# Performance work log

Measured on AMD Instinct MI355X. Metric: run time of the kernel, lower is better.

The kernel has to match this reference:

```python
import jax, jax.numpy as jnp
import numpy as np

D_MODEL, H, D_K = 768, 12, 64
B, S = 2, 2048
NEG = -1.0e9


def setup_inputs() -> dict:
    key = jax.random.key(0)
    ks = jax.random.split(key, 7)
    q = jax.random.normal(ks[0], (B, S, D_MODEL), dtype=jnp.float32)
    k = jax.random.normal(ks[1], (B, S, D_MODEL), dtype=jnp.float32)
    v = jax.random.normal(ks[2], (B, S, D_MODEL), dtype=jnp.float32)
    mask = jnp.tril(jnp.ones((S, S), dtype=jnp.int32))[None, None]  # [1,1,S,S] causal
    sc = 1.0 / np.sqrt(D_MODEL)
    w_q = jax.random.normal(ks[3], (D_MODEL, D_MODEL), dtype=jnp.float32) * sc
    w_k = jax.random.normal(ks[4], (D_MODEL, D_MODEL), dtype=jnp.float32) * sc
    w_v = jax.random.normal(ks[5], (D_MODEL, D_MODEL), dtype=jnp.float32) * sc
    w_o = jax.random.normal(ks[6], (D_MODEL, D_MODEL), dtype=jnp.float32) * sc
    return {"q": q, "k": k, "v": v, "mask": mask,
            "w_q": w_q, "w_k": w_k, "w_v": w_v, "w_o": w_o}


def reference(q, k, v, mask, w_q, w_k, w_v, w_o):
    # nn.Linear(x) = x @ W.T ; split heads: [B,S,D] -> [B,H,S,Dk]
    def split_heads(x, w):
        y = jnp.einsum('bsd,ed->bse', x, w)
        return y.reshape(x.shape[0], x.shape[1], H, D_K).transpose(0, 2, 1, 3)

    qh = split_heads(q, w_q)
    kh = split_heads(k, w_k)
    vh = split_heads(v, w_v)
    scores = jnp.einsum('bhqd,bhkd->bhqk', qh, kh) / jnp.sqrt(jnp.float32(D_K))
    scores = jnp.where(mask == 0, jnp.float32(NEG), scores)
    attn = jax.nn.softmax(scores, axis=-1)  # dropout p=0 -> identity
    ctx = jnp.einsum('bhqk,bhkd->bhqd', attn, vh)
    ctx = ctx.transpose(0, 2, 1, 3).reshape(q.shape[0], q.shape[1], D_MODEL)
    return jnp.einsum('bsd,ed->bse', ctx, w_o)
```

## Files before the change

kernel.cpp:

```cpp
#include <hip/hip_runtime.h>

#define DM   768
#define HN   12
#define DKH  64
#define BSZ  2
#define SEQ  2048
#define MROWS (BSZ*SEQ)
#define NEGBIG -1.0e9f
#define NSLOT 40
#define QSCALE 0.18033688011112042f

typedef __bf16 bf16;
typedef __bf16 bf16x8 __attribute__((ext_vector_type(8)));
typedef __bf16 bf16x4 __attribute__((ext_vector_type(4)));
typedef float  f32x4  __attribute__((ext_vector_type(4)));
typedef unsigned int uint32;

__device__ __forceinline__ void gload_lds16(const void* g, void* l) {
    __builtin_amdgcn_global_load_lds(
        (const __attribute__((address_space(1))) char*)g,
        (__attribute__((address_space(3))) char*)l, 16, 0, 0);
}

__global__ __launch_bounds__(256) void cvt4(const float* __restrict__ a, const float* __restrict__ b,
                                            const float* __restrict__ c, const float* __restrict__ e,
                                            bf16* __restrict__ x, bf16* __restrict__ y,
                                            bf16* __restrict__ z, bf16* __restrict__ u, int n) {
    const float* s; bf16* d;
    if      (blockIdx.y == 0) { s = a; d = x; }
    else if (blockIdx.y == 1) { s = b; d = y; }
    else if (blockIdx.y == 2) { s = c; d = z; }
    else                      { s = e; d = u; }
    int i = (blockIdx.x * 256 + threadIdx.x) * 4;
    if (i + 3 < n) {
        float4 v = *(const float4*)(s + i);
        bf16x4 o; o[0] = (bf16)v.x; o[1] = (bf16)v.y; o[2] = (bf16)v.z; o[3] = (bf16)v.w;
        *(bf16x4*)(d + i) = o;
    }
}

__global__ __launch_bounds__(256) void gemm_qkv(
    const float* __restrict__ xq, const float* __restrict__ xk, const float* __restrict__ xv,
    const bf16* __restrict__ wq, const bf16* __restrict__ wk, const bf16* __restrict__ wv,
    bf16* __restrict__ qh, bf16* __restrict__ kh, bf16* __restrict__ vt)
{
    __shared__ float Asf[128 * 32];
    __shared__ bf16  Bs[128 * 32];

    const float* A; const bf16* Bw; bf16* Out; float qs;
    if      (blockIdx.z == 0) { A = xq; Bw = wq; Out = qh; qs = QSCALE; }
    else if (blockIdx.z == 1) { A = xk; Bw = wk; Out = kh; qs = 1.0f; }
    else                      { A = xv; Bw = wv; Out = vt; qs = 1.0f; }
    const bool vout = (blockIdx.z == 2);

    const int t = threadIdx.x, w = t >> 6, lane = t & 63;
    const int g = lane >> 4, lo = lane & 15;
    const int mt = blockIdx.x * 128, nt = blockIdx.y * 128;
    const int wr = (w >> 1) * 64, wc = (w & 1) * 64;

    f32x4 acc[4][4] = {};

    for (int k0 = 0; k0 < DM; k0 += 32) {
        #pragma unroll
        for (int i = 0; i < 4; i++) {
            int c = i * 256 + t;
            int row = c >> 3, cc = (c & 7) ^ (row & 7);
            gload_lds16(A + (size_t)(mt + row) * DM + k0 + cc * 4, (char*)Asf + c * 16);
        }
        #pragma unroll
        for (int i = 0; i < 2; i++) {
            int c = i * 256 + t;
            int row = c >> 2, col = (c & 3) * 8;
            gload_lds16(Bw + (size_t)(nt + row) * DM + k0 + col, (char*)Bs + c * 16);
        }
        asm volatile("s_waitcnt vmcnt(0)" ::: "memory");
        __syncthreads();

        bf16x8 af[4], bfr[4];
        #pragma unroll
        for (int m = 0; m < 4; m++) {
            int row = wr + m * 16 + lo;
            const char* rp = (const char*)Asf + row * 128;
            float4 f0 = *(const float4*)(rp + (((2 * g)     ^ (lo & 7)) << 4));
            float4 f1 = *(const float4*)(rp + (((2 * g + 1) ^ (lo & 7)) << 4));
            bf16x8 a;
            a[0] = (bf16)f0.x; a[1] = (bf16)f0.y; a[2] = (bf16)f0.z; a[3] = (bf16)f0.w;
            a[4] = (bf16)f1.x; a[5] = (bf16)f1.y; a[6] = (bf16)f1.z; a[7] = (bf16)f1.w;
            af[m] = a;
        }
        #pragma unroll
        for (int n = 0; n < 4; n++)
            bfr[n] = *(const bf16x8*)&Bs[(wc + n * 16 + lo) * 32 + g * 8];
        #pragma unroll
        for (int m = 0; m < 4; m++)
            #pragma unroll
            for (int n = 0; n < 4; n++)
                acc[m][n] = __builtin_amdgcn_mfma_f32_16x16x32_bf16(af[m], bfr[n], acc[m][n], 0, 0, 0);
        __syncthreads();
    }

    if (!vout) {
        #pragma unroll
        for (int m = 0; m < 4; m++) {
            #pragma unroll
            for (int n = 0; n < 4; n++) {
                #pragma unroll
                for (int r = 0; r < 4; r++) {
                    int gm = mt + wr + m * 16 + g * 4 + r;
                    int gn = nt + wc + n * 16 + lo;
                    int b = gm >> 11, s = gm & 2047, h = gn >> 6, d = gn & 63;
                    Out[(((size_t)b * HN + h) * SEQ + s) * DKH + d] = (bf16)(acc[m][n][r] * qs);
                }
            }
        }
    } else {
        #pragma unroll
        for (int m = 0; m < 4; m++) {
            #pragma unroll
            for (int n = 0; n < 4; n++) {
                int gm = mt + wr + m * 16 + g * 4;
                int gn = nt + wc + n * 16 + lo;
                int b = gm >> 11, s0 = gm & 2047, h = gn >> 6, d = gn & 63;
                bf16x4 pk;
                #pragma unroll
                for (int r = 0; r < 4; r++) pk[r] = (bf16)acc[m][n][r];
                *(bf16x4*)&Out[(((size_t)b * HN + h) * DKH + d) * SEQ + s0] = pk;
            }
        }
    }
}

__global__ __launch_bounds__(256) void gemm_out(
    const bf16* __restrict__ Actx, const bf16* __restrict__ Bw, float* __restrict__ Out)
{
    __shared__ bf16 As[128 * 32];
    __shared__ bf16 Bs[128 * 32];

    const int t = threadIdx.x, w = t >> 6, lane = t & 63;
    const int mt = blockIdx.x * 128, nt = blockIdx.y * 128;
    const int wr = (w >> 1) * 64, wc = (w & 1) * 64;

    f32x4 acc[4][4] = {};

    for (int k0 = 0; k0 < DM; k0 += 32) {
        #pragma unroll
        for (int i = 0; i < 2; i++) {
            int c = i * 256 + t;
            int row = c >> 2, col = (c & 3) * 8;
            gload_lds16(Actx + (size_t)(mt + row) * DM + k0 + col, (char*)As + c * 16);
            gload_lds16(Bw   + (size_t)(nt + row) * DM + k0 + col, (char*)Bs + c * 16);
        }
        asm volatile("s_waitcnt vmcnt(0)" ::: "memory");
        __syncthreads();

        bf16x8 af[4], bfr[4];
        #pragma unroll
        for (int m = 0; m < 4; m++)
            af[m] = *(const bf16x8*)&As[(wr + m * 16 + (lane & 15)) * 32 + (lane >> 4) * 8];
        #pragma unroll
        for (int n = 0; n < 4; n++)
            bfr[n] = *(const bf16x8*)&Bs[(wc + n * 16 + (lane & 15)) * 32 + (lane >> 4) * 8];
        #pragma unroll
        for (int m = 0; m < 4; m++)
            #pragma unroll
            for (int n = 0; n < 4; n++)
                acc[m][n] = __builtin_amdgcn_mfma_f32_16x16x32_bf16(af[m], bfr[n], acc[m][n], 0, 0, 0);
        __syncthreads();
    }

    #pragma unroll
    for (int m = 0; m < 4; m++) {
        #pragma unroll
        for (int n = 0; n < 4; n++) {
            #pragma unroll
            for (int r = 0; r < 4; r++) {
                int gm = mt + wr + m * 16 + (lane >> 4) * 4 + r;
                int gn = nt + wc + n * 16 + (lane & 15);
                Out[(size_t)gm * DM + gn] = acc[m][n][r];
            }
        }
    }
}

__global__ __launch_bounds__(256, 4) void flash_split(
    const bf16* __restrict__ qh, const bf16* __restrict__ kh,
    const bf16* __restrict__ vt, bf16* __restrict__ ctx,
    bf16* __restrict__ pO, float* __restrict__ pM, float* __restrict__ pL)
{
    __shared__ bf16 Ks[2][4096];
    __shared__ bf16 Vs[2][4096];
    __shared__ bf16 pl[4][1024];

    const int bid = blockIdx.x;
    const int slot = bid / 24;
    const int bh = bid % 24;

    int qt, p, np;
    if (slot < 16)      { qt = 15 - (slot >> 2); p = slot & 3;  np = 4; }
    else if (slot < 28) { int s = slot - 16; qt = 11 - s / 3; p = s % 3; np = 3; }
    else if (slot < 36) { int s = slot - 28; qt = 7 - (s >> 1); p = s & 1; np = 2; }
    else                { qt = 39 - slot; p = 0; np = 1; }

    const int T = 2 * qt + 2;
    const int bse = T / np, rem = T - bse * np;
    const int cnt   = bse + (p < rem ? 1 : 0);
    const int start = p * bse + (p < rem ? p : rem);

    const int qb = qt * 128;
    const int t = threadIdx.x, w = t >> 6, lane = t & 63;
    const int g = lane >> 4, lo = lane & 15;
    const size_t base = (size_t)bh * SEQ * DKH;
    const char* khead = (const char*)(kh + base);
    const char* vhead = (const char*)(vt + base);

    uint32 koff[2], voff[2];
    #pragma unroll
    for (int i = 0; i < 2; i++) {
        int c = w * 128 + i * 64 + lane;
        int r = c >> 3, s = c & 7;
        int sw = s ^ (r & 7);
        koff[i] = (uint32)(r * 128  + 16 * sw);
        voff[i] = (uint32)(r * 4096 + 16 * sw);
    }
    const uint32 kr0 = (uint32)(128 * lo + 16 * (g ^ (lo & 7)));
    const uint32 kr1 = kr0 ^ 64;

    uint32 pw[4], pr[2];
    #pragma unroll
    for (int cg = 0; cg < 4; cg++)
        pw[cg] = (uint32)(lo * 128 + (((2 * cg + (g >> 1)) ^ (lo & 7)) << 4) + (g & 1) * 8);
    #pragma unroll
    for (int kq = 0; kq < 2; kq++)
        pr[kq] = (uint32)(lo * 128 + (((4 * kq + g) ^ (lo & 7)) << 4));
    char* plb = (char*)&pl[w][0];

    const int qrow0 = qb + 16 * w + lo;
    const int qrow1 = qb + 64 + 16 * w + lo;
    const bf16* qp0 = qh + base + (size_t)qrow0 * DKH + g * 8;
    const bf16* qp1 = qh + base + (size_t)qrow1 * DKH + g * 8;
    bf16x8 qa0 = *(const bf16x8*)qp0;
    bf16x8 qa1 = *(const bf16x8*)(qp0 + 32);
    bf16x8 qb0 = *(const bf16x8*)qp1;
    bf16x8 qb1 = *(const bf16x8*)(qp1 + 32);

    f32x4 O0[4] = {}, O1[4] = {};
    float m0 = -1e30f, l0 = 0.0f, m1 = -1e30f, l1 = 0.0f;

    #pragma unroll
    for (int i = 0; i < 2; i++) {
        int c16 = (w * 128 + i * 64 + lane) * 16;
        gload_lds16(khead + (size_t)start * 8192 + koff[i], (char*)&Ks[0][0] + c16);
        gload_lds16(vhead + (size_t)start * 128  + voff[i], (char*)&Vs[0][0] + c16);
    }
    asm volatile("s_waitcnt vmcnt(0)" ::: "memory");
    __syncthreads();

    for (int it = 0; it < cnt; ++it) {
        const int kt = start + it;
        const int par = it & 1, nxt = par ^ 1;
        if (it + 1 < cnt) {
            const char* ks = khead + (size_t)(kt + 1) * 8192;
            const char* vs = vhead + (size_t)(kt + 1) * 128;
            #pragma unroll
            for (int i = 0; i < 2; i++) {
                int c16 = (w * 128 + i * 64 + lane) * 16;
                gload_lds16(ks + koff[i], (char*)&Ks[nxt][0] + c16);
                gload_lds16(vs + voff[i], (char*)&Vs[nxt][0] + c16);
            }
        }

        const bool act0  = (kt != T - 1);
        const bool diag0 = (kt == T - 2);
        const bool diag1 = (kt == T - 1);

        const char* Kp = (const char*)&Ks[par][0];
        f32x4 s0[4], s1[4];
        {
            bf16x8 kf0[4], kf1[4];
            #pragma unroll
            for (int cg = 0; cg < 4; cg++) {
                kf0[cg] = *(const bf16x8*)(Kp + cg * 2048 + kr0);
                kf1[cg] = *(const bf16x8*)(Kp + cg * 2048 + kr1);
            }
            __builtin_amdgcn_s_setprio(1);
            if (act0) {
                #pragma unroll
                for (int cg = 0; cg < 4; cg++) {
                    f32x4 z = {0.0f, 0.0f, 0.0f, 0.0f};
                    z = __builtin_amdgcn_mfma_f32_16x16x32_bf16(kf0[cg], qa0, z, 0, 0, 0);
                    z = __builtin_amdgcn_mfma_f32_16x16x32_bf16(kf1[cg], qa1, z, 0, 0, 0);
                    s0[cg] = z;
                }
            }
            #pragma unroll
            for (int cg = 0; cg < 4; cg++) {
                f32x4 z = {0.0f, 0.0f, 0.0f, 0.0f};
                z = __builtin_amdgcn_mfma_f32_16x16x32_bf16(kf0[cg], qb0, z, 0, 0, 0);
                z = __builtin_amdgcn_mfma_f32_16x16x32_bf16(kf1[cg], qb1, z, 0, 0, 0);
                s1[cg] = z;
            }
            __builtin_amdgcn_s_setprio(0);
        }

        if (act0 && diag0) {
            #pragma unroll
            for (int cg = 0; cg < 4; cg++)
                #pragma unroll
                for (int r = 0; r < 4; r++) {
                    int ki = kt * 64 + cg * 16 + 4 * g + r;
                    s0[cg][r] = (ki > qrow0) ? NEGBIG : s0[cg][r];
                }
        }
        if (diag1) {
            #pragma unroll
            for (int cg = 0; cg < 4; cg++)
                #pragma unroll
                for (int r = 0; r < 4; r++) {
                    int ki = kt * 64 + cg * 16 + 4 * g + r;
                    s1[cg][r] = (ki > qrow1) ? NEGBIG : s1[cg][r];
                }
        }

        if (act0) {
            float mx = fmaxf(fmaxf(fmaxf(s0[0][0], s0[0][1]), fmaxf(s0[0][2], s0[0][3])),
                             fmaxf(fmaxf(s0[1][0], s0[1][1]), fmaxf(s0[1][2], s0[1][3])));
            mx = fmaxf(mx, fmaxf(fmaxf(fmaxf(s0[2][0], s0[2][1]), fmaxf(s0[2][2], s0[2][3])),
                                 fmaxf(fmaxf(s0[3][0], s0[3][1]), fmaxf(s0[3][2], s0[3][3]))));
            mx = fmaxf(mx, __shfl_xor(mx, 16, 64));
            mx = fmaxf(mx, __shfl_xor(mx, 32, 64));
            if (!__all(mx - m0 <= 8.0f)) {
                float mnew = fmaxf(m0, mx);
                float scl = __builtin_exp2f(m0 - mnew);
                m0 = mnew; l0 *= scl;
                float s4[4];
                #pragma unroll
                for (int r = 0; r < 4; r++) s4[r] = __shfl(scl, 4 * g + r, 64);
                #pragma unroll
                for (int dg = 0; dg < 4; dg++)
                    #pragma unroll
                    for (int r = 0; r < 4; r++) O0[dg][r] *= s4[r];
            }
            float rs = 0.0f;
            #pragma unroll
            for (int cg = 0; cg < 4; cg++)
                #pragma unroll
                for (int r = 0; r < 4; r++) {
                    s0[cg][r] = __builtin_exp2f(s0[cg][r] - m0);
                    rs += s0[cg][r];
                }
            rs += __shfl_xor(rs, 16, 64);
            rs += __shfl_xor(rs, 32, 64);
            l0 += rs;
        }
        {
            float mx = fmaxf(fmaxf(fmaxf(s1[0][0], s1[0][1]), fmaxf(s1[0][2], s1[0][3])),
                             fmaxf(fmaxf(s1[1][0], s1[1][1]), fmaxf(s1[1][2], s1[1][3])));
            mx = fmaxf(mx, fmaxf(fmaxf(fmaxf(s1[2][0], s1[2][1]), fmaxf(s1[2][2], s1[2][3])),
                                 fmaxf(fmaxf(s1[3][0], s1[3][1]), fmaxf(s1[3][2], s1[3][3]))));
            mx = fmaxf(mx, __shfl_xor(mx, 16, 64));
            mx = fmaxf(mx, __shfl_xor(mx, 32, 64));
            if (!__all(mx - m1 <= 8.0f)) {
                float mnew = fmaxf(m1, mx);
                float scl = __builtin_exp2f(m1 - mnew);
                m1 = mnew; l1 *= scl;
                float s4[4];
                #pragma unroll
                for (int r = 0; r < 4; r++) s4[r] = __shfl(scl, 4 * g + r, 64);
                #pragma unroll
                for (int dg = 0; dg < 4; dg++)
                    #pragma unroll
                    for (int r = 0; r < 4; r++) O1[dg][r] *= s4[r];
            }
            float rs = 0.0f;
            #pragma unroll
            for (int cg = 0; cg < 4; cg++)
                #pragma unroll
                for (int r = 0; r < 4; r++) {
                    s1[cg][r] = __builtin_exp2f(s1[cg][r] - m1);
                    rs += s1[cg][r];
                }
            rs += __shfl_xor(rs, 16, 64);
            rs += __shfl_xor(rs, 32, 64);
            l1 += rs;
        }

        const char* Vp = (const char*)&Vs[par][0];
        bf16x8 vv[8];
        #pragma unroll
        for (int kq = 0; kq < 2; kq++)
            #pragma unroll
            for (int dblk = 0; dblk < 4; dblk++)
                vv[kq * 4 + dblk] = *(const bf16x8*)
                    (Vp + (dblk * 16 + lo) * 128 + 16 * ((4 * kq + g) ^ (lo & 7)));

        if (act0) {
            #pragma unroll
            for (int cg = 0; cg < 4; cg++) {
                bf16x4 pk;
                #pragma unroll
                for (int r = 0; r < 4; r++) pk[r] = (bf16)s0[cg][r];
                *(bf16x4*)(plb + pw[cg]) = pk;
            }
        }
        asm volatile("s_waitcnt lgkmcnt(0)" ::: "memory");
        __builtin_amdgcn_sched_barrier(0);
        if (act0) {
            __builtin_amdgcn_s_setprio(1);
            #pragma unroll
            for (int kq = 0; kq < 2; kq++) {
                bf16x8 pa = *(const bf16x8*)(plb + pr[kq]);
                #pragma unroll
                for (int dblk = 0; dblk < 4; dblk++)
                    O0[dblk] = __builtin_amdgcn_mfma_f32_16x16x32_bf16(pa, vv[kq * 4 + dblk], O0[dblk], 0, 0, 0);
            }
            __builtin_amdgcn_s_setprio(0);
        }
        __builtin_amdgcn_sched_barrier(0);
        {
            #pragma unroll
            for (int cg = 0; cg < 4; cg++) {
                bf16x4 pk;
                #pragma unroll
                for (int r = 0; r < 4; r++) pk[r] = (bf16)s1[cg][r];
                *(bf16x4*)(plb + pw[cg]) = pk;
            }
            asm volatile("s_waitcnt lgkmcnt(0)" ::: "memory");
            __builtin_amdgcn_sched_barrier(0);
            __builtin_amdgcn_s_setprio(1);
            #pragma unroll
            for (int kq = 0; kq < 2; kq++) {
                bf16x8 pa = *(const bf16x8*)(plb + pr[kq]);
                #pragma unroll
                for (int dblk = 0; dblk < 4; dblk++)
                    O1[dblk] = __builtin_amdgcn_mfma_f32_16x16x32_bf16(pa, vv[kq * 4 + dblk], O1[dblk], 0, 0, 0);
            }
            __builtin_amdgcn_s_setprio(0);
        }

        asm volatile("s_waitcnt vmcnt(0)" ::: "memory");
        __syncthreads();
    }

    if (np == 1) {
        const int b = bh / HN, h = bh % HN;
        float inv0[4], inv1[4];
        #pragma unroll
        for (int r = 0; r < 4; r++) {
            inv0[r] = 1.0f / __shfl(l0, 4 * g + r, 64);
            inv1[r] = 1.0f / __shfl(l1, 4 * g + r, 64);
        }
        #pragma unroll
        for (int dg = 0; dg < 4; dg++) {
            #pragma unroll
            for (int r = 0; r < 4; r++) {
                int row0 = qb + 16 * w + g * 4 + r;
                int row1 = qb + 64 + 16 * w + g * 4 + r;
                ctx[((size_t)(b * SEQ + row0)) * DM + h * DKH + dg * 16 + lo] =
                    (bf16)(O0[dg][r] * inv0[r]);
                ctx[((size_t)(b * SEQ + row1)) * DM + h * DKH + dg * 16 + lo] =
                    (bf16)(O1[dg][r] * inv1[r]);
            }
        }
    } else {
        const int pslot = bh * NSLOT + slot;
        bf16* po = pO + (size_t)pslot * 128 * 64;
        #pragma unroll
        for (int dg = 0; dg < 4; dg++) {
            #pragma unroll
            for (int r = 0; r < 4; r++) {
                int r0 = 16 * w + 4 * g + r;
                po[r0 * 64 + dg * 16 + lo]        = (bf16)O0[dg][r];
                po[(64 + r0) * 64 + dg * 16 + lo] = (bf16)O1[dg][r];
            }
        }
        if (g == 0) {
            pM[pslot * 128 + 16 * w + lo]      = m0;
            pL[pslot * 128 + 16 * w + lo]      = l0;
            pM[pslot * 128 + 64 + 16 * w + lo] = m1;
            pL[pslot * 128 + 64 + 16 * w + lo] = l1;
        }
    }
}

__global__ __launch_bounds__(256) void flash_combine(
    const bf16* __restrict__ pO, const float* __restrict__ pM,
    const float* __restrict__ pL, bf16* __restrict__ ctx)
{
    const int bh = blockIdx.x;
    const int qt = 4 + blockIdx.y;
    int np, s0;
    if (qt >= 12)     { np = 4; s0 = (15 - qt) * 4; }
    else if (qt >= 8) { np = 3; s0 = 16 + (11 - qt) * 3; }
    else              { np = 2; s0 = 28 + (7 - qt) * 2; }

    const int t = threadIdx.x;
    const int row = t >> 1, dh = (t & 1) * 32;
    const int pbase = bh * NSLOT + s0;

    float mi[4], wi[4];
    float mstar = -1e30f;
    #pragma unroll
    for (int i = 0; i < 4; i++)
        if (i < np) { mi[i] = pM[(pbase + i) * 128 + row]; mstar = fmaxf(mstar, mi[i]); }
    float lsum = 0.0f;
    #pragma unroll
    for (int i = 0; i < 4; i++)
        if (i < np) { wi[i] = __builtin_exp2f(mi[i] - mstar); lsum += wi[i] * pL[(pbase + i) * 128 + row]; }
    const float linv = 1.0f / lsum;

    const int b = bh / HN, h = bh % HN;
    bf16* crow = ctx + ((size_t)(b * SEQ + qt * 128 + row)) * DM + h * DKH + dh;

    #pragma unroll
    for (int d0 = 0; d0 < 32; d0 += 8) {
        float acc[8] = {};
        #pragma unroll
        for (int i = 0; i < 4; i++) {
            if (i < np) {
                bf16x8 o = *(const bf16x8*)&pO[((size_t)(pbase + i) * 128 + row) * 64 + dh + d0];
                #pragma unroll
                for (int j = 0; j < 8; j++) acc[j] += wi[i] * (float)o[j];
            }
        }
        bf16x8 ov;
        #pragma unroll
        for (int j = 0; j < 8; j++) ov[j] = (bf16)(acc[j] * linv);
        *(bf16x8*)(crow + d0) = ov;
    }
}

extern "C" void kernel_launch(void* const* d_in, const int* in_sizes, int n_in,
                              void* d_out, int out_size, void* d_ws, size_t ws_size,
                              hipStream_t stream) {
    const float* q  = (const float*)d_in[0];
    const float* k  = (const float*)d_in[1];
    const float* v  = (const float*)d_in[2];
    const float* wq = (const float*)d_in[4];
    const float* wk = (const float*)d_in[5];
    const float* wv = (const float*)d_in[6];
    const float* wo = (const float*)d_in[7];
    float* out = (float*)d_out;

    const size_t NX = (size_t)MROWS * DM;
    const size_t NW = (size_t)DM * DM;

    bf16* p = (bf16*)d_ws;
    bf16* wqb = p; p += NW;
    bf16* wkb = p; p += NW;
    bf16* wvb = p; p += NW;
    bf16* wob = p; p += NW;
    bf16* qhp = p; p += NX;
    bf16* khp = p; p += NX;
    bf16* vtp = p; p += NX;
    bf16* ctxp = p; p += NX;
    bf16* pO = p; p += (size_t)24 * NSLOT * 128 * 64;
    float* pM = (float*)p;
    float* pL = pM + 24 * NSLOT * 128;

    cvt4<<<dim3(NW / 1024, 4), 256, 0, stream>>>(wq, wk, wv, wo, wqb, wkb, wvb, wob, (int)NW);

    gemm_qkv<<<dim3(MROWS / 128, DM / 128, 3), 256, 0, stream>>>(
        q, k, v, wqb, wkb, wvb, qhp, khp, vtp);

    flash_split<<<24 * NSLOT, 256, 0, stream>>>(qhp, khp, vtp, ctxp, pO, pM, pL);
    flash_combine<<<dim3(24, 12), 256, 0, stream>>>(pO, pM, pL, ctxp);

    gemm_out<<<dim3(MROWS / 128, DM / 128), 256, 0, stream>>>(ctxp, wob, out);
}
```

Before: 118.5 us.

## Fuse weight fp32-to-bf16 conversion into GEMM tile loads, drop cvt4 kernel

Removes the separate weight conversion kernel and has the QKV and output GEMMs load fp32 weight tiles into LDS (swizzled like the activation tiles) and convert to bf16 in registers. This saves one kernel launch and the round trip of the converted weights through memory. In exchange it doubles LDS traffic and footprint for the B tiles and adds conversion work inside every k-step. It also lowers the flash_split occupancy hint from 4 to 3 blocks per CU.

```diff
diff --git a/kernel.cpp b/kernel.cpp
--- a/kernel.cpp
+++ b/kernel.cpp
@@ -22,32 +22,15 @@
         (__attribute__((address_space(3))) char*)l, 16, 0, 0);
 }
 
-__global__ __launch_bounds__(256) void cvt4(const float* __restrict__ a, const float* __restrict__ b,
-                                            const float* __restrict__ c, const float* __restrict__ e,
-                                            bf16* __restrict__ x, bf16* __restrict__ y,
-                                            bf16* __restrict__ z, bf16* __restrict__ u, int n) {
-    const float* s; bf16* d;
-    if      (blockIdx.y == 0) { s = a; d = x; }
-    else if (blockIdx.y == 1) { s = b; d = y; }
-    else if (blockIdx.y == 2) { s = c; d = z; }
-    else                      { s = e; d = u; }
-    int i = (blockIdx.x * 256 + threadIdx.x) * 4;
-    if (i + 3 < n) {
-        float4 v = *(const float4*)(s + i);
-        bf16x4 o; o[0] = (bf16)v.x; o[1] = (bf16)v.y; o[2] = (bf16)v.z; o[3] = (bf16)v.w;
-        *(bf16x4*)(d + i) = o;
-    }
-}
-
 __global__ __launch_bounds__(256) void gemm_qkv(
     const float* __restrict__ xq, const float* __restrict__ xk, const float* __restrict__ xv,
-    const bf16* __restrict__ wq, const bf16* __restrict__ wk, const bf16* __restrict__ wv,
+    const float* __restrict__ wq, const float* __restrict__ wk, const float* __restrict__ wv,
     bf16* __restrict__ qh, bf16* __restrict__ kh, bf16* __restrict__ vt)
 {
     __shared__ float Asf[128 * 32];
-    __shared__ bf16  Bs[128 * 32];
-
-    const float* A; const bf16* Bw; bf16* Out; float qs;
+    __shared__ float Bsf[128 * 32];
+
+    const float* A; const float* Bw; bf16* Out; float qs;
     if      (blockIdx.z == 0) { A = xq; Bw = wq; Out = qh; qs = QSCALE; }
     else if (blockIdx.z == 1) { A = xk; Bw = wk; Out = kh; qs = 1.0f; }
     else                      { A = xv; Bw = wv; Out = vt; qs = 1.0f; }
@@ -65,13 +48,8 @@
         for (int i = 0; i < 4; i++) {
             int c = i * 256 + t;
             int row = c >> 3, cc = (c & 7) ^ (row & 7);
-            gload_lds16(A + (size_t)(mt + row) * DM + k0 + cc * 4, (char*)Asf + c * 16);
-        }
-        #pragma unroll
-        for (int i = 0; i < 2; i++) {
-            int c = i * 256 + t;
-            int row = c >> 2, col = (c & 3) * 8;
-            gload_lds16(Bw + (size_t)(nt + row) * DM + k0 + col, (char*)Bs + c * 16);
+            gload_lds16(A  + (size_t)(mt + row) * DM + k0 + cc * 4, (char*)Asf + c * 16);
+            gload_lds16(Bw + (size_t)(nt + row) * DM + k0 + cc * 4, (char*)Bsf + c * 16);
         }
         asm volatile("s_waitcnt vmcnt(0)" ::: "memory");
         __syncthreads();
@@ -79,8 +57,7 @@
         bf16x8 af[4], bfr[4];
         #pragma unroll
         for (int m = 0; m < 4; m++) {
-            int row = wr + m * 16 + lo;
-            const char* rp = (const char*)Asf + row * 128;
+            const char* rp = (const char*)Asf + (wr + m * 16 + lo) * 128;
             float4 f0 = *(const float4*)(rp + (((2 * g)     ^ (lo & 7)) << 4));
             float4 f1 = *(const float4*)(rp + (((2 * g + 1) ^ (lo & 7)) << 4));
             bf16x8 a;
@@ -89,8 +66,15 @@
             af[m] = a;
         }
         #pragma unroll
-        for (int n = 0; n < 4; n++)
-            bfr[n] = *(const bf16x8*)&Bs[(wc + n * 16 + lo) * 32 + g * 8];
+        for (int n = 0; n < 4; n++) {
+            const char* rp = (const char*)Bsf + (wc + n * 16 + lo) * 128;
+            float4 f0 = *(const float4*)(rp + (((2 * g)     ^ (lo & 7)) << 4));
+            float4 f1 = *(const float4*)(rp + (((2 * g + 1) ^ (lo & 7)) << 4));
+            bf16x8 b;
+            b[0] = (bf16)f0.x; b[1] = (bf16)f0.y; b[2] = (bf16)f0.z; b[3] = (bf16)f0.w;
+            b[4] = (bf16)f1.x; b[5] = (bf16)f1.y; b[6] = (bf16)f1.z; b[7] = (bf16)f1.w;
+            bfr[n] = b;
+        }
         #pragma unroll
         for (int m = 0; m < 4; m++)
             #pragma unroll
@@ -131,12 +115,13 @@
 }
 
 __global__ __launch_bounds__(256) void gemm_out(
-    const bf16* __restrict__ Actx, const bf16* __restrict__ Bw, float* __restrict__ Out)
+    const bf16* __restrict__ Actx, const float* __restrict__ Bw, float* __restrict__ Out)
 {
-    __shared__ bf16 As[128 * 32];
-    __shared__ bf16 Bs[128 * 32];
+    __shared__ bf16  As[128 * 32];
+    __shared__ float Bsf[128 * 32];
 
     const int t = threadIdx.x, w = t >> 6, lane = t & 63;
+    const int g = lane >> 4, lo = lane & 15;
     const int mt = blockIdx.x * 128, nt = blockIdx.y * 128;
     const int wr = (w >> 1) * 64, wc = (w & 1) * 64;
 
@@ -148,7 +133,12 @@
             int c = i * 256 + t;
             int row = c >> 2, col = (c & 3) * 8;
             gload_lds16(Actx + (size_t)(mt + row) * DM + k0 + col, (char*)As + c * 16);
-            gload_lds16(Bw   + (size_t)(nt + row) * DM + k0 + col, (char*)Bs + c * 16);
+        }
+        #pragma unroll
+        for (int i = 0; i < 4; i++) {
+            int c = i * 256 + t;
+            int row = c >> 3, cc = (c & 7) ^ (row & 7);
+            gload_lds16(Bw + (size_t)(nt + row) * DM + k0 + cc * 4, (char*)Bsf + c * 16);
         }
         asm volatile("s_waitcnt vmcnt(0)" ::: "memory");
         __syncthreads();
@@ -156,10 +146,17 @@
         bf16x8 af[4], bfr[4];
         #pragma unroll
         for (int m = 0; m < 4; m++)
-            af[m] = *(const bf16x8*)&As[(wr + m * 16 + (lane & 15)) * 32 + (lane >> 4) * 8];
-        #pragma unroll
-        for (int n = 0; n < 4; n++)
-            bfr[n] = *(const bf16x8*)&Bs[(wc + n * 16 + (lane & 15)) * 32 + (lane >> 4) * 8];
+            af[m] = *(const bf16x8*)&As[(wr + m * 16 + lo) * 32 + g * 8];
+        #pragma unroll
+        for (int n = 0; n < 4; n++) {
+            const char* rp = (const char*)Bsf + (wc + n * 16 + lo) * 128;
+            float4 f0 = *(const float4*)(rp + (((2 * g)     ^ (lo & 7)) << 4));
+            float4 f1 = *(const float4*)(rp + (((2 * g + 1) ^ (lo & 7)) << 4));
+            bf16x8 b;
+            b[0] = (bf16)f0.x; b[1] = (bf16)f0.y; b[2] = (bf16)f0.z; b[3] = (bf16)f0.w;
+            b[4] = (bf16)f1.x; b[5] = (bf16)f1.y; b[6] = (bf16)f1.z; b[7] = (bf16)f1.w;
+            bfr[n] = b;
+        }
         #pragma unroll
         for (int m = 0; m < 4; m++)
             #pragma unroll
@@ -174,15 +171,15 @@
         for (int n = 0; n < 4; n++) {
             #pragma unroll
             for (int r = 0; r < 4; r++) {
-                int gm = mt + wr + m * 16 + (lane >> 4) * 4 + r;
-                int gn = nt + wc + n * 16 + (lane & 15);
+                int gm = mt + wr + m * 16 + g * 4 + r;
+                int gn = nt + wc + n * 16 + lo;
                 Out[(size_t)gm * DM + gn] = acc[m][n][r];
             }
         }
     }
 }
 
-__global__ __launch_bounds__(256, 4) void flash_split(
+__global__ __launch_bounds__(256, 3) void flash_split(
     const bf16* __restrict__ qh, const bf16* __restrict__ kh,
     const bf16* __restrict__ vt, bf16* __restrict__ ctx,
     bf16* __restrict__ pO, float* __restrict__ pM, float* __restrict__ pL)
@@ -542,13 +539,8 @@
     float* out = (float*)d_out;
 
     const size_t NX = (size_t)MROWS * DM;
-    const size_t NW = (size_t)DM * DM;
 
     bf16* p = (bf16*)d_ws;
-    bf16* wqb = p; p += NW;
-    bf16* wkb = p; p += NW;
-    bf16* wvb = p; p += NW;
-    bf16* wob = p; p += NW;
     bf16* qhp = p; p += NX;
     bf16* khp = p; p += NX;
     bf16* vtp = p; p += NX;
@@ -557,13 +549,11 @@
     float* pM = (float*)p;
     float* pL = pM + 24 * NSLOT * 128;
 
-    cvt4<<<dim3(NW / 1024, 4), 256, 0, stream>>>(wq, wk, wv, wo, wqb, wkb, wvb, wob, (int)NW);
-
     gemm_qkv<<<dim3(MROWS / 128, DM / 128, 3), 256, 0, stream>>>(
-        q, k, v, wqb, wkb, wvb, qhp, khp, vtp);
+        q, k, v, wq, wk, wv, qhp, khp, vtp);
 
     flash_split<<<24 * NSLOT, 256, 0, stream>>>(qhp, khp, vtp, ctxp, pO, pM, pL);
     flash_combine<<<dim3(24, 12), 256, 0, stream>>>(pO, pM, pL, ctxp);
 
-    gemm_out<<<dim3(MROWS / 128, DM / 128), 256, 0, stream>>>(ctxp, wob, out);
+    gemm_out<<<dim3(MROWS / 128, DM / 128), 256, 0, stream>>>(ctxp, wo, out);
 }
```

After: 116.3 us. No clear change (-1.8%).

## Double-buffer GEMM tiles and convert output weights to bf16 on the fly in LDS

Applied to the files above, without the earlier changes.

Both projection GEMMs now keep two LDS buffers and issue the next k-tile's global-to-LDS loads before computing the current one, so load latency overlaps with MFMA work. The output projection reads fp32 w_o directly through a swizzled LDS layout and converts it to bf16 during fragment loads, which drops the fourth conversion pass and its workspace. The flash kernel's launch-bounds occupancy hint is lowered from 4 to 3 blocks. The extra buffers double LDS use per GEMM block, which may reduce how many blocks fit on each CU.

```diff
diff --git a/kernel.cpp b/kernel.cpp
--- a/kernel.cpp
+++ b/kernel.cpp
@@ -44,8 +44,8 @@
     const bf16* __restrict__ wq, const bf16* __restrict__ wk, const bf16* __restrict__ wv,
     bf16* __restrict__ qh, bf16* __restrict__ kh, bf16* __restrict__ vt)
 {
-    __shared__ float Asf[128 * 32];
-    __shared__ bf16  Bs[128 * 32];
+    __shared__ float Asf[2][128 * 32];
+    __shared__ bf16  Bs[2][128 * 32];
 
     const float* A; const bf16* Bw; bf16* Out; float qs;
     if      (blockIdx.z == 0) { A = xq; Bw = wq; Out = qh; qs = QSCALE; }
@@ -60,27 +60,45 @@
 
     f32x4 acc[4][4] = {};
 
-    for (int k0 = 0; k0 < DM; k0 += 32) {
-        #pragma unroll
-        for (int i = 0; i < 4; i++) {
-            int c = i * 256 + t;
-            int row = c >> 3, cc = (c & 7) ^ (row & 7);
-            gload_lds16(A + (size_t)(mt + row) * DM + k0 + cc * 4, (char*)Asf + c * 16);
-        }
-        #pragma unroll
-        for (int i = 0; i < 2; i++) {
-            int c = i * 256 + t;
-            int row = c >> 2, col = (c & 3) * 8;
-            gload_lds16(Bw + (size_t)(nt + row) * DM + k0 + col, (char*)Bs + c * 16);
-        }
-        asm volatile("s_waitcnt vmcnt(0)" ::: "memory");
-        __syncthreads();
+    const int NT = DM / 32;
+
+    #pragma unroll
+    for (int i = 0; i < 4; i++) {
+        int c = i * 256 + t;
+        int row = c >> 3, cc = (c & 7) ^ (row & 7);
+        gload_lds16(A + (size_t)(mt + row) * DM + cc * 4, (char*)&Asf[0][0] + c * 16);
+    }
+    #pragma unroll
+    for (int i = 0; i < 2; i++) {
+        int c = i * 256 + t;
+        int row = c >> 2, col = (c & 3) * 8;
+        gload_lds16(Bw + (size_t)(nt + row) * DM + col, (char*)&Bs[0][0] + c * 16);
+    }
+    asm volatile("s_waitcnt vmcnt(0)" ::: "memory");
+    __syncthreads();
+
+    for (int it = 0; it < NT; ++it) {
+        const int par = it & 1, nxt = par ^ 1;
+        if (it + 1 < NT) {
+            int k0 = (it + 1) * 32;
+            #pragma unroll
+            for (int i = 0; i < 4; i++) {
+                int c = i * 256 + t;
+                int row = c >> 3, cc = (c & 7) ^ (row & 7);
+                gload_lds16(A + (size_t)(mt + row) * DM + k0 + cc * 4, (char*)&Asf[nxt][0] + c * 16);
+            }
+            #pragma unroll
+            for (int i = 0; i < 2; i++) {
+                int c = i * 256 + t;
+                int row = c >> 2, col = (c & 3) * 8;
+                gload_lds16(Bw + (size_t)(nt + row) * DM + k0 + col, (char*)&Bs[nxt][0] + c * 16);
+            }
+        }
 
         bf16x8 af[4], bfr[4];
         #pragma unroll
         for (int m = 0; m < 4; m++) {
-            int row = wr + m * 16 + lo;
-            const char* rp = (const char*)Asf + row * 128;
+            const char* rp = (const char*)&Asf[par][0] + (wr + m * 16 + lo) * 128;
             float4 f0 = *(const float4*)(rp + (((2 * g)     ^ (lo & 7)) << 4));
             float4 f1 = *(const float4*)(rp + (((2 * g + 1) ^ (lo & 7)) << 4));
             bf16x8 a;
@@ -90,12 +108,14 @@
         }
         #pragma unroll
         for (int n = 0; n < 4; n++)
-            bfr[n] = *(const bf16x8*)&Bs[(wc + n * 16 + lo) * 32 + g * 8];
+            bfr[n] = *(const bf16x8*)&Bs[par][(wc + n * 16 + lo) * 32 + g * 8];
         #pragma unroll
         for (int m = 0; m < 4; m++)
             #pragma unroll
             for (int n = 0; n < 4; n++)
                 acc[m][n] = __builtin_amdgcn_mfma_f32_16x16x32_bf16(af[m], bfr[n], acc[m][n], 0, 0, 0);
+
+        asm volatile("s_waitcnt vmcnt(0)" ::: "memory");
         __syncthreads();
     }
 
@@ -131,41 +151,74 @@
 }
 
 __global__ __launch_bounds__(256) void gemm_out(
-    const bf16* __restrict__ Actx, const bf16* __restrict__ Bw, float* __restrict__ Out)
+    const bf16* __restrict__ Actx, const float* __restrict__ Bw, float* __restrict__ Out)
 {
-    __shared__ bf16 As[128 * 32];
-    __shared__ bf16 Bs[128 * 32];
+    __shared__ bf16  As[2][128 * 32];
+    __shared__ float Bsf[2][128 * 32];
 
     const int t = threadIdx.x, w = t >> 6, lane = t & 63;
+    const int g = lane >> 4, lo = lane & 15;
     const int mt = blockIdx.x * 128, nt = blockIdx.y * 128;
     const int wr = (w >> 1) * 64, wc = (w & 1) * 64;
 
     f32x4 acc[4][4] = {};
-
-    for (int k0 = 0; k0 < DM; k0 += 32) {
-        #pragma unroll
-        for (int i = 0; i < 2; i++) {
-            int c = i * 256 + t;
-            int row = c >> 2, col = (c & 3) * 8;
-            gload_lds16(Actx + (size_t)(mt + row) * DM + k0 + col, (char*)As + c * 16);
-            gload_lds16(Bw   + (size_t)(nt + row) * DM + k0 + col, (char*)Bs + c * 16);
-        }
+    const int NT = DM / 32;
+
+    #pragma unroll
+    for (int i = 0; i < 2; i++) {
+        int c = i * 256 + t;
+        int row = c >> 2, col = (c & 3) * 8;
+        gload_lds16(Actx + (size_t)(mt + row) * DM + col, (char*)&As[0][0] + c * 16);
+    }
+    #pragma unroll
+    for (int i = 0; i < 4; i++) {
+        int c = i * 256 + t;
+        int row = c >> 3, cc = (c & 7) ^ (row & 7);
+        gload_lds16(Bw + (size_t)(nt + row) * DM + cc * 4, (char*)&Bsf[0][0] + c * 16);
+    }
+    asm volatile("s_waitcnt vmcnt(0)" ::: "memory");
+    __syncthreads();
+
+    for (int it = 0; it < NT; ++it) {
+        const int par = it & 1, nxt = par ^ 1;
+        if (it + 1 < NT) {
+            int k0 = (it + 1) * 32;
+            #pragma unroll
+            for (int i = 0; i < 2; i++) {
+                int c = i * 256 + t;
+                int row = c >> 2, col = (c & 3) * 8;
+                gload_lds16(Actx + (size_t)(mt + row) * DM + k0 + col, (char*)&As[nxt][0] + c * 16);
+            }
+            #pragma unroll
+            for (int i = 0; i < 4; i++) {
+                int c = i * 256 + t;
+                int row = c >> 3, cc = (c & 7) ^ (row & 7);
+                gload_lds16(Bw + (size_t)(nt + row) * DM + k0 + cc * 4, (char*)&Bsf[nxt][0] + c * 16);
+            }
+        }
+
+        bf16x8 af[4], bfr[4];
+        #pragma unroll
+        for (int m = 0; m < 4; m++)
+            af[m] = *(const bf16x8*)&As[par][(wr + m * 16 + lo) * 32 + g * 8];
+        #pragma unroll
+        for (int n = 0; n < 4; n++) {
+            const char* rp = (const char*)&Bsf[par][0] + (wc + n * 16 + lo) * 128;
+            float4 f0 = *(const float4*)(rp + (((2 * g)     ^ (lo & 7)) << 4));
+            float4 f1 = *(const float4*)(rp + (((2 * g + 1) ^ (lo & 7)) << 4));
+            bf16x8 b;
+            b[0] = (bf16)f0.x; b[1] = (bf16)f0.y; b[2] = (bf16)f0.z; b[3] = (bf16)f0.w;
+            b[4] = (bf16)f1.x; b[5] = (bf16)f1.y; b[6] = (bf16)f1.z; b[7] = (bf16)f1.w;
+            bfr[n] = b;
+        }
+        #pragma unroll
+        for (int m = 0; m < 4; m++)
+            #pragma unroll
+            for (int n = 0; n < 4; n++)
+                acc[m][n] = __builtin_amdgcn_mfma_f32_16x16x32_bf16(af[m], bfr[n], acc[m][n], 0, 0, 0);
+
         asm volatile("s_waitcnt vmcnt(0)" ::: "memory");
         __syncthreads();
-
-        bf16x8 af[4], bfr[4];
-        #pragma unroll
-        for (int m = 0; m < 4; m++)
-            af[m] = *(const bf16x8*)&As[(wr + m * 16 + (lane & 15)) * 32 + (lane >> 4) * 8];
-        #pragma unroll
-        for (int n = 0; n < 4; n++)
-            bfr[n] = *(const bf16x8*)&Bs[(wc + n * 16 + (lane & 15)) * 32 + (lane >> 4) * 8];
-        #pragma unroll
-        for (int m = 0; m < 4; m++)
-            #pragma unroll
-            for (int n = 0; n < 4; n++)
-                acc[m][n] = __builtin_amdgcn_mfma_f32_16x16x32_bf16(af[m], bfr[n], acc[m][n], 0, 0, 0);
-        __syncthreads();
     }
 
     #pragma unroll
@@ -174,15 +227,15 @@
         for (int n = 0; n < 4; n++) {
             #pragma unroll
             for (int r = 0; r < 4; r++) {
-                int gm = mt + wr + m * 16 + (lane >> 4) * 4 + r;
-                int gn = nt + wc + n * 16 + (lane & 15);
+                int gm = mt + wr + m * 16 + g * 4 + r;
+                int gn = nt + wc + n * 16 + lo;
                 Out[(size_t)gm * DM + gn] = acc[m][n][r];
             }
         }
     }
 }
 
-__global__ __launch_bounds__(256, 4) void flash_split(
+__global__ __launch_bounds__(256, 3) void flash_split(
     const bf16* __restrict__ qh, const bf16* __restrict__ kh,
     const bf16* __restrict__ vt, bf16* __restrict__ ctx,
     bf16* __restrict__ pO, float* __restrict__ pM, float* __restrict__ pL)
@@ -548,7 +601,6 @@
     bf16* wqb = p; p += NW;
     bf16* wkb = p; p += NW;
     bf16* wvb = p; p += NW;
-    bf16* wob = p; p += NW;
     bf16* qhp = p; p += NX;
     bf16* khp = p; p += NX;
     bf16* vtp = p; p += NX;
@@ -557,7 +609,7 @@
     float* pM = (float*)p;
     float* pL = pM + 24 * NSLOT * 128;
 
-    cvt4<<<dim3(NW / 1024, 4), 256, 0, stream>>>(wq, wk, wv, wo, wqb, wkb, wvb, wob, (int)NW);
+    cvt4<<<dim3(NW / 1024, 3), 256, 0, stream>>>(wq, wk, wv, wq, wqb, wkb, wvb, wqb, (int)NW);
 
     gemm_qkv<<<dim3(MROWS / 128, DM / 128, 3), 256, 0, stream>>>(
         q, k, v, wqb, wkb, wvb, qhp, khp, vtp);
@@ -565,5 +617,5 @@
     flash_split<<<24 * NSLOT, 256, 0, stream>>>(qhp, khp, vtp, ctxp, pO, pM, pL);
     flash_combine<<<dim3(24, 12), 256, 0, stream>>>(pO, pM, pL, ctxp);
 
-    gemm_out<<<dim3(MROWS / 128, DM / 128), 256, 0, stream>>>(ctxp, wob, out);
+    gemm_out<<<dim3(MROWS / 128, DM / 128), 256, 0, stream>>>(ctxp, wo, out);
 }
```

Result: slower. 121.9 us (+2.9%).
